# Kernel tuning notes

Measured on AMD Instinct MI355X. Metric: run time of the kernel, lower is better.

The kernel has to match this reference:

```python
import jax, jax.numpy as jnp
import numpy as np

DIN = 1024
DIM = 1024
NUM_HEADS = 16
HEAD_DIM = DIM // NUM_HEADS
SEQ_LEN = 2048
BATCH = 2


def setup_inputs() -> dict:
    key = jax.random.key(0)
    ks = jax.random.split(key, 5)
    s = 0.02
    x = jax.random.normal(ks[0], (BATCH, SEQ_LEN, DIN), dtype=jnp.float32)
    # torch nn.Linear weights are (out_features, in_features)
    wq = jax.random.normal(ks[1], (DIM, DIN), dtype=jnp.float32) * s
    wk = jax.random.normal(ks[2], (DIM, DIN), dtype=jnp.float32) * s
    wv = jax.random.normal(ks[3], (DIM, DIN), dtype=jnp.float32) * s
    wo = jax.random.normal(ks[4], (DIM, DIM), dtype=jnp.float32) * s
    return {"x": x, "wq": wq, "wk": wk, "wv": wv, "wo": wo}


def reference(x, wq, wk, wv, wo):
    bs, seq_len, _ = x.shape
    # project and split heads: [b, h, s, d]
    def split(z):
        return z.reshape(bs, seq_len, NUM_HEADS, HEAD_DIM).transpose(0, 2, 1, 3)
    q = split(x @ wq.T)
    k = split(x @ wk.T)
    v = split(x @ wv.T)
    # raw scores, causal mask applied BEFORE the 1/sqrt(d) scaling (as in source;
    # -inf is invariant to positive scaling so math matches standard causal attn)
    att = jnp.einsum('bhqd,bhkd->bhqk', q, k)
    causal = jnp.triu(jnp.ones((seq_len, seq_len), dtype=bool), k=1)
    att = jnp.where(causal, -jnp.inf, att)
    att = jax.nn.softmax(att / jnp.sqrt(jnp.float32(HEAD_DIM)), axis=-1)
    ctx = jnp.einsum('bhqk,bhkd->bhqd', att, v)
    ctx = ctx.transpose(0, 2, 1, 3).reshape(bs, seq_len, DIM)
    return ctx @ wo.T
```

## Files before the change

kernel.cpp:

```cpp
#include <hip/hip_runtime.h>
#include <stdint.h>

#define DIN 1024
#define DIMM 1024
#define NH 16
#define HD 64
#define SEQ 2048
#define BATCH 2
#define MTOT (BATCH*SEQ)
#define LDP 72
#define SCALE 0.125f

typedef __bf16 bf16;
typedef __bf16 bf16x8 __attribute__((ext_vector_type(8)));
typedef __bf16 bf16x4 __attribute__((ext_vector_type(4)));
typedef float f32x4 __attribute__((ext_vector_type(4)));

__device__ __forceinline__ void async16(bf16* lds, const bf16* g) {
  __builtin_amdgcn_global_load_lds(
      (const __attribute__((address_space(1))) void*)g,
      (__attribute__((address_space(3))) void*)lds, 16, 0, 0);
}

__global__ __launch_bounds__(256) void convert_all(const float* __restrict__ x,
                                                   const float* __restrict__ wq,
                                                   const float* __restrict__ wk,
                                                   const float* __restrict__ wv,
                                                   const float* __restrict__ wo,
                                                   bf16* __restrict__ xb,
                                                   bf16* __restrict__ Wb) {
  const int t = blockIdx.x * 256 + threadIdx.x;
#pragma unroll
  for (int i = 0; i < 4; ++i) {
    const int c = t + i * 262144;
    const float* src;
    bf16* dst;
    if (c < 524288) {
      src = x + (size_t)c * 8;
      dst = xb + (size_t)c * 8;
    } else {
      const int cw = c - 524288;
      const int w = cw >> 17;
      const int off = (cw & 131071) * 8;
      const float* wp = (w == 0) ? wq : (w == 1) ? wk : (w == 2) ? wv : wo;
      src = wp + off;
      dst = Wb + (size_t)w * 1048576 + off;
    }
    f32x4 a = *(const f32x4*)src;
    f32x4 b = *(const f32x4*)(src + 4);
    bf16x8 r;
    r[0] = (bf16)a[0]; r[1] = (bf16)a[1]; r[2] = (bf16)a[2]; r[3] = (bf16)a[3];
    r[4] = (bf16)b[0]; r[5] = (bf16)b[1]; r[6] = (bf16)b[2]; r[7] = (bf16)b[3];
    *(bf16x8*)dst = r;
  }
}

__device__ __forceinline__ void mm128_core(const bf16* __restrict__ A,
                                           const bf16* __restrict__ B,
                                           int K, int mbase, int nbase,
                                           bf16* As, bf16* Bs,
                                           f32x4 acc[4][4]) {
  const int tid  = threadIdx.x;
  const int lane = tid & 63;
  const int wave = tid >> 6;
  const int lrow = lane & 15;
  const int quad = lane >> 4;
  const int wr = (wave >> 1) * 64;
  const int wc = (wave & 1) * 64;
  const int srow = tid >> 3;
  const int scol = (tid & 7) * 8;
  const int sx   = (((tid & 7) ^ (srow & 7))) * 8;

  for (int k0 = 0; k0 < K; k0 += 64) {
#pragma unroll
    for (int i = 0; i < 4; ++i) {
      async16(&As[(i * 32 + srow) * 64 + scol],
              &A[(size_t)(mbase + i * 32 + srow) * K + k0 + sx]);
      async16(&Bs[(i * 32 + srow) * 64 + scol],
              &B[(size_t)(nbase + i * 32 + srow) * K + k0 + sx]);
    }
    __syncthreads();
#pragma unroll
    for (int h = 0; h < 2; ++h) {
      const int cx = ((h * 4 + quad) ^ (lrow & 7)) * 8;
      bf16x8 af[4], bfr[4];
#pragma unroll
      for (int i = 0; i < 4; ++i) {
        af[i]  = *(const bf16x8*)&As[(wr + i * 16 + lrow) * 64 + cx];
        bfr[i] = *(const bf16x8*)&Bs[(wc + i * 16 + lrow) * 64 + cx];
      }
#pragma unroll
      for (int mt = 0; mt < 4; ++mt)
#pragma unroll
        for (int nt = 0; nt < 4; ++nt)
          acc[mt][nt] = __builtin_amdgcn_mfma_f32_16x16x32_bf16(af[mt], bfr[nt], acc[mt][nt], 0, 0, 0);
    }
    __syncthreads();
  }
}

__global__ __launch_bounds__(256) void qkv_gemm(const bf16* __restrict__ A,
                                                const bf16* __restrict__ B,
                                                bf16* __restrict__ Q,
                                                bf16* __restrict__ Kb,
                                                bf16* __restrict__ Vt) {
  __shared__ bf16 As[128 * 64];
  __shared__ bf16 Bs[128 * 64];
  const int lane = threadIdx.x & 63;
  const int wave = threadIdx.x >> 6;
  const int lrow = lane & 15;
  const int quad = lane >> 4;
  const int wr = (wave >> 1) * 64;
  const int wc = (wave & 1) * 64;
  const int lin = blockIdx.x;
  const int xcd = lin & 7;
  const int idx = lin >> 3;
  const int nbase = (xcd * 3 + idx % 3) * 128;
  const int mbase = (idx / 3) * 128;

  f32x4 acc[4][4] = {};
  mm128_core(A, B, DIN, mbase, nbase, As, Bs, acc);

#pragma unroll
  for (int mt = 0; mt < 4; ++mt) {
    const int m0 = mbase + wr + mt * 16 + quad * 4;
#pragma unroll
    for (int nt = 0; nt < 4; ++nt) {
      const int n16 = nbase + wc + nt * 16;
      const int n = n16 + lrow;
      if (n16 < 1024) {
#pragma unroll
        for (int rr = 0; rr < 4; ++rr)
          Q[(size_t)(m0 + rr) * 1024 + n] = (bf16)acc[mt][nt][rr];
      } else if (n16 < 2048) {
#pragma unroll
        for (int rr = 0; rr < 4; ++rr)
          Kb[(size_t)(m0 + rr) * 1024 + (n - 1024)] = (bf16)acc[mt][nt][rr];
      } else {
        const int nn = n - 2048;
        const int row = ((m0 >> 11) * 16 + (nn >> 6)) * 64 + (nn & 63);
        bf16x4 ov;
#pragma unroll
        for (int rr = 0; rr < 4; ++rr) ov[rr] = (bf16)acc[mt][nt][rr];
        *(bf16x4*)&Vt[(size_t)row * SEQ + (m0 & 2047)] = ov;
      }
    }
  }
}

__global__ __launch_bounds__(256) void proj_gemm(const bf16* __restrict__ A,
                                                 const bf16* __restrict__ B,
                                                 float* __restrict__ C) {
  __shared__ bf16 As[128 * 64];
  __shared__ bf16 Bs[64 * 64];
  const int tid  = threadIdx.x;
  const int lane = tid & 63;
  const int wave = tid >> 6;
  const int lrow = lane & 15;
  const int quad = lane >> 4;
  const int wr = (wave >> 1) * 64;
  const int wc = (wave & 1) * 32;
  const int lin = blockIdx.x;
  const int xcd = lin & 7;
  const int idx = lin >> 3;
  const int nbase = (xcd * 2 + (idx & 1)) * 64;
  const int mbase = (idx >> 1) * 128;
  const int srow = tid >> 3;
  const int scol = (tid & 7) * 8;
  const int sx   = ((tid & 7) ^ (srow & 7)) * 8;

  f32x4 acc[4][2] = {};

  for (int k0 = 0; k0 < DIMM; k0 += 64) {
#pragma unroll
    for (int i = 0; i < 4; ++i)
      async16(&As[(i * 32 + srow) * 64 + scol],
              &A[(size_t)(mbase + i * 32 + srow) * DIMM + k0 + sx]);
#pragma unroll
    for (int i = 0; i < 2; ++i)
      async16(&Bs[(i * 32 + srow) * 64 + scol],
              &B[(size_t)(nbase + i * 32 + srow) * DIMM + k0 + sx]);
    __syncthreads();
#pragma unroll
    for (int h = 0; h < 2; ++h) {
      const int cx = ((h * 4 + quad) ^ (lrow & 7)) * 8;
      bf16x8 af[4], bfr[2];
#pragma unroll
      for (int i = 0; i < 4; ++i)
        af[i] = *(const bf16x8*)&As[(wr + i * 16 + lrow) * 64 + cx];
#pragma unroll
      for (int i = 0; i < 2; ++i)
        bfr[i] = *(const bf16x8*)&Bs[(wc + i * 16 + lrow) * 64 + cx];
#pragma unroll
      for (int mt = 0; mt < 4; ++mt)
#pragma unroll
        for (int nt = 0; nt < 2; ++nt)
          acc[mt][nt] = __builtin_amdgcn_mfma_f32_16x16x32_bf16(af[mt], bfr[nt], acc[mt][nt], 0, 0, 0);
    }
    __syncthreads();
  }

#pragma unroll
  for (int mt = 0; mt < 4; ++mt) {
    const int m0 = mbase + wr + mt * 16 + quad * 4;
#pragma unroll
    for (int nt = 0; nt < 2; ++nt) {
      const int n = nbase + wc + nt * 16 + lrow;
#pragma unroll
      for (int rr = 0; rr < 4; ++rr)
        C[(size_t)(m0 + rr) * 1024 + n] = acc[mt][nt][rr];
    }
  }
}

__global__ __launch_bounds__(512, 4) void attn(const bf16* __restrict__ Q,
                                               const bf16* __restrict__ K,
                                               const bf16* __restrict__ Vt,
                                               bf16* __restrict__ O) {
  __shared__ bf16 Ks[2][64 * 64];
  __shared__ bf16 Vts[2][64 * 64];
  __shared__ bf16 Plds[8][16 * LDP];
  const int tid  = threadIdx.x;
  const int wave = tid >> 6;
  const int lane = tid & 63;
  const int lrow = lane & 15;
  const int quad = lane >> 4;
  const int bh = blockIdx.x & 31;
  const int g  = blockIdx.x >> 5;
  const int qc = (g < 8) ? g : 23 - g;
  const int b  = bh >> 4;
  const int h  = bh & 15;
  const int qw = qc * 128 + wave * 16;
  const int ntiles = 2 * qc + 2;

  const bf16* Qh  = Q  + (size_t)(b * SEQ) * DIMM + h * HD;
  const bf16* Kh  = K  + (size_t)(b * SEQ) * DIMM + h * HD;
  const bf16* Vth = Vt + (size_t)bh * 64 * SEQ;
  bf16* Pw = Plds[wave];

  const int srow = tid >> 3;
  const int scol = (tid & 7) * 8;
  const int sx   = ((tid & 7) ^ (srow & 7)) * 8;
  const int cx0 = ((0 + quad) ^ (lrow & 7)) * 8;
  const int cx1 = ((4 + quad) ^ (lrow & 7)) * 8;

  bf16x8 qf0 = *(const bf16x8*)&Qh[(size_t)(qw + lrow) * DIMM + quad * 8];
  bf16x8 qf1 = *(const bf16x8*)&Qh[(size_t)(qw + lrow) * DIMM + 32 + quad * 8];

  async16(&Ks[0][srow * 64 + scol],  &Kh[(size_t)srow * DIMM + sx]);
  async16(&Vts[0][srow * 64 + scol], &Vth[(size_t)srow * SEQ + sx]);
  __syncthreads();

  float m_i = -1e30f, l_i = 0.f;
  f32x4 o_acc[4] = {};
  int cur = 0;

  for (int kt = 0; kt < ntiles; ++kt) {
    const int kbase = kt * 64;
    if (kt + 1 < ntiles) {
      const int nb = kbase + 64;
      async16(&Ks[cur ^ 1][srow * 64 + scol],  &Kh[(size_t)(nb + srow) * DIMM + sx]);
      async16(&Vts[cur ^ 1][srow * 64 + scol], &Vth[(size_t)srow * SEQ + nb + sx]);
    }
    if (kbase <= qw + 15) {
      const bf16* Kc = Ks[cur];
      const bf16* Vc = Vts[cur];
      f32x4 s[4] = {};
#pragma unroll
      for (int gg = 0; gg < 4; ++gg) {
        bf16x8 kf0 = *(const bf16x8*)&Kc[(gg * 16 + lrow) * 64 + cx0];
        bf16x8 kf1 = *(const bf16x8*)&Kc[(gg * 16 + lrow) * 64 + cx1];
        s[gg] = __builtin_amdgcn_mfma_f32_16x16x32_bf16(kf0, qf0, s[gg], 0, 0, 0);
        s[gg] = __builtin_amdgcn_mfma_f32_16x16x32_bf16(kf1, qf1, s[gg], 0, 0, 0);
      }
      if (kbase + 63 > qw) {
        const int qrow = qw + lrow;
#pragma unroll
        for (int gg = 0; gg < 4; ++gg)
#pragma unroll
          for (int r = 0; r < 4; ++r)
            s[gg][r] = (kbase + gg * 16 + quad * 4 + r > qrow) ? -1e30f : s[gg][r];
      }
      float pm = s[0][0];
#pragma unroll
      for (int gg = 0; gg < 4; ++gg)
#pragma unroll
        for (int r = 0; r < 4; ++r) pm = fmaxf(pm, s[gg][r]);
      pm = fmaxf(pm, __shfl_xor(pm, 16));
      pm = fmaxf(pm, __shfl_xor(pm, 32));
      const float mn = fmaxf(m_i, pm);
      const float al = __expf((m_i - mn) * SCALE);
      float sum = 0.f;
#pragma unroll
      for (int gg = 0; gg < 4; ++gg) {
        bf16x4 pk;
#pragma unroll
        for (int r = 0; r < 4; ++r) {
          const float p = __expf((s[gg][r] - mn) * SCALE);
          sum += p;
          pk[r] = (bf16)p;
        }
        *(bf16x4*)&Pw[lrow * LDP + gg * 16 + quad * 4] = pk;
      }
      sum += __shfl_xor(sum, 16);
      sum += __shfl_xor(sum, 32);
      l_i = l_i * al + sum;
      m_i = mn;
#pragma unroll
      for (int dt = 0; dt < 4; ++dt)
#pragma unroll
        for (int r = 0; r < 4; ++r)
          o_acc[dt][r] *= al;
      bf16x8 vf[8];
#pragma unroll
      for (int dt = 0; dt < 4; ++dt) {
        vf[2 * dt]     = *(const bf16x8*)&Vc[(dt * 16 + lrow) * 64 + cx0];
        vf[2 * dt + 1] = *(const bf16x8*)&Vc[(dt * 16 + lrow) * 64 + cx1];
      }
      bf16x8 pf0 = *(const bf16x8*)&Pw[lrow * LDP + quad * 8];
      bf16x8 pf1 = *(const bf16x8*)&Pw[lrow * LDP + 32 + quad * 8];
#pragma unroll
      for (int dt = 0; dt < 4; ++dt) {
        o_acc[dt] = __builtin_amdgcn_mfma_f32_16x16x32_bf16(vf[2 * dt],     pf0, o_acc[dt], 0, 0, 0);
        o_acc[dt] = __builtin_amdgcn_mfma_f32_16x16x32_bf16(vf[2 * dt + 1], pf1, o_acc[dt], 0, 0, 0);
      }
    }
    __syncthreads();
    cur ^= 1;
  }

  const float rl = __builtin_amdgcn_rcpf(l_i);
  bf16* Ob = O + (size_t)(b * SEQ + qw + lrow) * DIMM + h * HD;
#pragma unroll
  for (int dt = 0; dt < 4; ++dt) {
    bf16x4 ov;
#pragma unroll
    for (int r = 0; r < 4; ++r)
      ov[r] = (bf16)(o_acc[dt][r] * rl);
    *(bf16x4*)&Ob[dt * 16 + quad * 4] = ov;
  }
}

extern "C" void kernel_launch(void* const* d_in, const int* in_sizes, int n_in,
                              void* d_out, int out_size, void* d_ws, size_t ws_size,
                              hipStream_t stream) {
  const float* x  = (const float*)d_in[0];
  const float* wq = (const float*)d_in[1];
  const float* wk = (const float*)d_in[2];
  const float* wv = (const float*)d_in[3];
  const float* wo = (const float*)d_in[4];

  const size_t M4 = (size_t)MTOT * DIMM;
  bf16* xb  = (bf16*)d_ws;
  bf16* Wb  = xb + M4;
  bf16* Q   = Wb + M4;
  bf16* Kb  = Q + M4;
  bf16* Vt  = Kb + M4;
  bf16* CTX = xb;
  float* out = (float*)d_out;

  convert_all<<<dim3(1024), dim3(256), 0, stream>>>(x, wq, wk, wv, wo, xb, Wb);
  qkv_gemm<<<dim3(768), dim3(256), 0, stream>>>(xb, Wb, Q, Kb, Vt);
  attn<<<dim3(BATCH * NH * (SEQ / 128)), dim3(512), 0, stream>>>(Q, Kb, Vt, CTX);
  proj_gemm<<<dim3(512), dim3(256), 0, stream>>>(CTX, Wb + 3 * 1048576, out);
}
```

Before: 188.8 us.

## Restructure attention: 64-row blocks, register-resident P, lazy rescale, exp2

```diff
diff --git a/kernel.cpp b/kernel.cpp
--- a/kernel.cpp
+++ b/kernel.cpp
@@ -8,7 +8,6 @@
 #define SEQ 2048
 #define BATCH 2
 #define MTOT (BATCH*SEQ)
-#define LDP 72
 #define SCALE 0.125f
 
 typedef __bf16 bf16;
@@ -213,117 +212,130 @@
   }
 }
 
-__global__ __launch_bounds__(512, 4) void attn(const bf16* __restrict__ Q,
+__global__ __launch_bounds__(256, 4) void attn(const bf16* __restrict__ Q,
                                                const bf16* __restrict__ K,
                                                const bf16* __restrict__ Vt,
                                                bf16* __restrict__ O) {
   __shared__ bf16 Ks[2][64 * 64];
   __shared__ bf16 Vts[2][64 * 64];
-  __shared__ bf16 Plds[8][16 * LDP];
   const int tid  = threadIdx.x;
   const int wave = tid >> 6;
   const int lane = tid & 63;
   const int lrow = lane & 15;
   const int quad = lane >> 4;
-  const int bh = blockIdx.x & 31;
-  const int g  = blockIdx.x >> 5;
-  const int qc = (g < 8) ? g : 23 - g;
-  const int b  = bh >> 4;
-  const int h  = bh & 15;
-  const int qw = qc * 128 + wave * 16;
-  const int ntiles = 2 * qc + 2;
+  const int lin  = blockIdx.x;
+  const int bh   = lin & 31;
+  const int j    = lin >> 5;
+  const int t    = j & 7;
+  const int grp  = j >> 3;
+  const int qi   = (grp == 0) ? (31 - t) : (grp == 1) ? t
+                 : (grp == 2) ? (23 - t) : (8 + t);
+  const int b = bh >> 4;
+  const int h = bh & 15;
+  const int qb = qi * 64;
+  const int qw = qb + wave * 16;
+  const int ntiles = qi + 1;
 
   const bf16* Qh  = Q  + (size_t)(b * SEQ) * DIMM + h * HD;
   const bf16* Kh  = K  + (size_t)(b * SEQ) * DIMM + h * HD;
   const bf16* Vth = Vt + (size_t)bh * 64 * SEQ;
-  bf16* Pw = Plds[wave];
 
   const int srow = tid >> 3;
   const int scol = (tid & 7) * 8;
   const int sx   = ((tid & 7) ^ (srow & 7)) * 8;
   const int cx0 = ((0 + quad) ^ (lrow & 7)) * 8;
   const int cx1 = ((4 + quad) ^ (lrow & 7)) * 8;
+  const int LL = lrow & 7;
+  const int qh = quad >> 1, ql = quad & 1;
+  int vc[4];
+#pragma unroll
+  for (int g = 0; g < 4; ++g)
+    vc[g] = ((((2 * g + qh) ^ LL) << 1) | ql) * 4;
 
   bf16x8 qf0 = *(const bf16x8*)&Qh[(size_t)(qw + lrow) * DIMM + quad * 8];
   bf16x8 qf1 = *(const bf16x8*)&Qh[(size_t)(qw + lrow) * DIMM + 32 + quad * 8];
 
-  async16(&Ks[0][srow * 64 + scol],  &Kh[(size_t)srow * DIMM + sx]);
-  async16(&Vts[0][srow * 64 + scol], &Vth[(size_t)srow * SEQ + sx]);
+  async16(&Ks[0][srow * 64 + scol],         &Kh[(size_t)srow * DIMM + sx]);
+  async16(&Ks[0][(srow + 32) * 64 + scol],  &Kh[(size_t)(srow + 32) * DIMM + sx]);
+  async16(&Vts[0][srow * 64 + scol],        &Vth[(size_t)srow * SEQ + sx]);
+  async16(&Vts[0][(srow + 32) * 64 + scol], &Vth[(size_t)(srow + 32) * SEQ + sx]);
   __syncthreads();
 
   float m_i = -1e30f, l_i = 0.f;
   f32x4 o_acc[4] = {};
   int cur = 0;
+  const float C1 = 0.18033688f;
 
   for (int kt = 0; kt < ntiles; ++kt) {
     const int kbase = kt * 64;
     if (kt + 1 < ntiles) {
       const int nb = kbase + 64;
-      async16(&Ks[cur ^ 1][srow * 64 + scol],  &Kh[(size_t)(nb + srow) * DIMM + sx]);
-      async16(&Vts[cur ^ 1][srow * 64 + scol], &Vth[(size_t)srow * SEQ + nb + sx]);
-    }
-    if (kbase <= qw + 15) {
-      const bf16* Kc = Ks[cur];
-      const bf16* Vc = Vts[cur];
-      f32x4 s[4] = {};
-#pragma unroll
-      for (int gg = 0; gg < 4; ++gg) {
-        bf16x8 kf0 = *(const bf16x8*)&Kc[(gg * 16 + lrow) * 64 + cx0];
-        bf16x8 kf1 = *(const bf16x8*)&Kc[(gg * 16 + lrow) * 64 + cx1];
-        s[gg] = __builtin_amdgcn_mfma_f32_16x16x32_bf16(kf0, qf0, s[gg], 0, 0, 0);
-        s[gg] = __builtin_amdgcn_mfma_f32_16x16x32_bf16(kf1, qf1, s[gg], 0, 0, 0);
+      async16(&Ks[cur ^ 1][srow * 64 + scol],         &Kh[(size_t)(nb + srow) * DIMM + sx]);
+      async16(&Ks[cur ^ 1][(srow + 32) * 64 + scol],  &Kh[(size_t)(nb + srow + 32) * DIMM + sx]);
+      async16(&Vts[cur ^ 1][srow * 64 + scol],        &Vth[(size_t)srow * SEQ + nb + sx]);
+      async16(&Vts[cur ^ 1][(srow + 32) * 64 + scol], &Vth[(size_t)(srow + 32) * SEQ + nb + sx]);
+    }
+    const bf16* Kc = Ks[cur];
+    const bf16* Vc = Vts[cur];
+    f32x4 s[4] = {};
+#pragma unroll
+    for (int gg = 0; gg < 4; ++gg) {
+      bf16x8 kf0 = *(const bf16x8*)&Kc[(gg * 16 + lrow) * 64 + cx0];
+      bf16x8 kf1 = *(const bf16x8*)&Kc[(gg * 16 + lrow) * 64 + cx1];
+      s[gg] = __builtin_amdgcn_mfma_f32_16x16x32_bf16(kf0, qf0, s[gg], 0, 0, 0);
+      s[gg] = __builtin_amdgcn_mfma_f32_16x16x32_bf16(kf1, qf1, s[gg], 0, 0, 0);
+    }
+    if (kbase + 63 > qw) {
+      const int qrow = qw + lrow;
+#pragma unroll
+      for (int gg = 0; gg < 4; ++gg)
+#pragma unroll
+        for (int r = 0; r < 4; ++r)
+          s[gg][r] = (kbase + gg * 16 + quad * 4 + r > qrow) ? -1e30f : s[gg][r];
+    }
+    float pm = s[0][0];
+#pragma unroll
+    for (int gg = 0; gg < 4; ++gg)
+#pragma unroll
+      for (int r = 0; r < 4; ++r) pm = fmaxf(pm, s[gg][r]);
+    pm = fmaxf(pm, __shfl_xor(pm, 16));
+    pm = fmaxf(pm, __shfl_xor(pm, 32));
+    if (!__all(pm - m_i <= 64.f)) {
+      const float mn = fmaxf(m_i, pm);
+      const float al = __builtin_amdgcn_exp2f((m_i - mn) * C1);
+      l_i *= al;
+#pragma unroll
+      for (int dt = 0; dt < 4; ++dt)
+#pragma unroll
+        for (int r = 0; r < 4; ++r) o_acc[dt][r] *= al;
+      m_i = mn;
+    }
+    const float mnc = m_i * C1;
+    float sum = 0.f;
+    bf16x8 pf0, pf1;
+#pragma unroll
+    for (int gg = 0; gg < 4; ++gg)
+#pragma unroll
+      for (int r = 0; r < 4; ++r) {
+        const float p = __builtin_amdgcn_exp2f(fmaf(s[gg][r], C1, -mnc));
+        sum += p;
+        if (gg < 2) pf0[(gg & 1) * 4 + r] = (bf16)p;
+        else        pf1[(gg & 1) * 4 + r] = (bf16)p;
       }
-      if (kbase + 63 > qw) {
-        const int qrow = qw + lrow;
-#pragma unroll
-        for (int gg = 0; gg < 4; ++gg)
-#pragma unroll
-          for (int r = 0; r < 4; ++r)
-            s[gg][r] = (kbase + gg * 16 + quad * 4 + r > qrow) ? -1e30f : s[gg][r];
-      }
-      float pm = s[0][0];
-#pragma unroll
-      for (int gg = 0; gg < 4; ++gg)
-#pragma unroll
-        for (int r = 0; r < 4; ++r) pm = fmaxf(pm, s[gg][r]);
-      pm = fmaxf(pm, __shfl_xor(pm, 16));
-      pm = fmaxf(pm, __shfl_xor(pm, 32));
-      const float mn = fmaxf(m_i, pm);
-      const float al = __expf((m_i - mn) * SCALE);
-      float sum = 0.f;
-#pragma unroll
-      for (int gg = 0; gg < 4; ++gg) {
-        bf16x4 pk;
-#pragma unroll
-        for (int r = 0; r < 4; ++r) {
-          const float p = __expf((s[gg][r] - mn) * SCALE);
-          sum += p;
-          pk[r] = (bf16)p;
-        }
-        *(bf16x4*)&Pw[lrow * LDP + gg * 16 + quad * 4] = pk;
-      }
-      sum += __shfl_xor(sum, 16);
-      sum += __shfl_xor(sum, 32);
-      l_i = l_i * al + sum;
-      m_i = mn;
-#pragma unroll
-      for (int dt = 0; dt < 4; ++dt)
-#pragma unroll
-        for (int r = 0; r < 4; ++r)
-          o_acc[dt][r] *= al;
-      bf16x8 vf[8];
-#pragma unroll
-      for (int dt = 0; dt < 4; ++dt) {
-        vf[2 * dt]     = *(const bf16x8*)&Vc[(dt * 16 + lrow) * 64 + cx0];
-        vf[2 * dt + 1] = *(const bf16x8*)&Vc[(dt * 16 + lrow) * 64 + cx1];
-      }
-      bf16x8 pf0 = *(const bf16x8*)&Pw[lrow * LDP + quad * 8];
-      bf16x8 pf1 = *(const bf16x8*)&Pw[lrow * LDP + 32 + quad * 8];
-#pragma unroll
-      for (int dt = 0; dt < 4; ++dt) {
-        o_acc[dt] = __builtin_amdgcn_mfma_f32_16x16x32_bf16(vf[2 * dt],     pf0, o_acc[dt], 0, 0, 0);
-        o_acc[dt] = __builtin_amdgcn_mfma_f32_16x16x32_bf16(vf[2 * dt + 1], pf1, o_acc[dt], 0, 0, 0);
-      }
+    sum += __shfl_xor(sum, 16);
+    sum += __shfl_xor(sum, 32);
+    l_i += sum;
+#pragma unroll
+    for (int dt = 0; dt < 4; ++dt) {
+      const bf16* Vr = &Vc[(dt * 16 + lrow) * 64];
+      bf16x4 a0 = *(const bf16x4*)&Vr[vc[0]];
+      bf16x4 a1 = *(const bf16x4*)&Vr[vc[1]];
+      bf16x4 b0 = *(const bf16x4*)&Vr[vc[2]];
+      bf16x4 b1 = *(const bf16x4*)&Vr[vc[3]];
+      bf16x8 vfA = __builtin_shufflevector(a0, a1, 0, 1, 2, 3, 4, 5, 6, 7);
+      bf16x8 vfB = __builtin_shufflevector(b0, b1, 0, 1, 2, 3, 4, 5, 6, 7);
+      o_acc[dt] = __builtin_amdgcn_mfma_f32_16x16x32_bf16(vfA, pf0, o_acc[dt], 0, 0, 0);
+      o_acc[dt] = __builtin_amdgcn_mfma_f32_16x16x32_bf16(vfB, pf1, o_acc[dt], 0, 0, 0);
     }
     __syncthreads();
     cur ^= 1;
@@ -361,6 +373,6 @@
 
   convert_all<<<dim3(1024), dim3(256), 0, stream>>>(x, wq, wk, wv, wo, xb, Wb);
   qkv_gemm<<<dim3(768), dim3(256), 0, stream>>>(xb, Wb, Q, Kb, Vt);
-  attn<<<dim3(BATCH * NH * (SEQ / 128)), dim3(512), 0, stream>>>(Q, Kb, Vt, CTX);
+  attn<<<dim3(BATCH * NH * (SEQ / 64)), dim3(256), 0, stream>>>(Q, Kb, Vt, CTX);
   proj_gemm<<<dim3(512), dim3(256), 0, stream>>>(CTX, Wb + 3 * 1048576, out);
 }
```

New measurement: 183.5 us. 1.03x faster.
